# Optimization experiments

Hardware: AMD Instinct MI355X
Metric: run time of the kernel (lower is better)

## Reference

```python
import jax, jax.numpy as jnp
import numpy as np

N_NODES = 50000
N_EDGES = 800000
IN_DIM = 128
HID = 128
EMB = 128
HORIZON = 64
ACT = 8
N_AGENTS = 1024


def setup_inputs() -> dict:
    key = jax.random.key(0)
    ks = jax.random.split(key, 16)
    sc = lambda fan_in: 1.0 / np.sqrt(fan_in)

    inp = {
        "node_features": jax.random.normal(ks[0], (N_NODES, IN_DIM), dtype=jnp.float32),
        "edge_index": jax.random.randint(ks[1], (2, N_EDGES), 0, N_NODES, dtype=jnp.int64),
        "agent_idx": jax.random.randint(ks[2], (N_AGENTS,), 0, N_NODES, dtype=jnp.int64),
        # GraphConv1: out = lin_rel(sum_j x_j) + lin_root(x); lin_root has no bias
        "W1_rel": jax.random.uniform(ks[3], (HID, IN_DIM), jnp.float32, -sc(IN_DIM), sc(IN_DIM)),
        "b1_rel": jax.random.uniform(ks[4], (HID,), jnp.float32, -sc(IN_DIM), sc(IN_DIM)),
        "W1_root": jax.random.uniform(ks[5], (HID, IN_DIM), jnp.float32, -sc(IN_DIM), sc(IN_DIM)),
        # GraphConv2
        "W2_rel": jax.random.uniform(ks[6], (EMB, HID), jnp.float32, -sc(HID), sc(HID)),
        "b2_rel": jax.random.uniform(ks[7], (EMB,), jnp.float32, -sc(HID), sc(HID)),
        "W2_root": jax.random.uniform(ks[8], (EMB, HID), jnp.float32, -sc(HID), sc(HID)),
        # Policy MLP: Linear(EMB,HID)-ReLU-Linear(HID,HID)-ReLU-Linear(HID,HORIZON*ACT)
        "Wp1": jax.random.uniform(ks[9], (HID, EMB), jnp.float32, -sc(EMB), sc(EMB)),
        "bp1": jax.random.uniform(ks[10], (HID,), jnp.float32, -sc(EMB), sc(EMB)),
        "Wp2": jax.random.uniform(ks[11], (HID, HID), jnp.float32, -sc(HID), sc(HID)),
        "bp2": jax.random.uniform(ks[12], (HID,), jnp.float32, -sc(HID), sc(HID)),
        "Wp3": jax.random.uniform(ks[13], (HORIZON * ACT, HID), jnp.float32, -sc(HID), sc(HID)),
        "bp3": jax.random.uniform(ks[14], (HORIZON * ACT,), jnp.float32, -sc(HID), sc(HID)),
    }
    return inp


def _graph_conv(x, src, dst, W_rel, b_rel, W_root):
    # aggregate neighbor features (sum over incoming edges), then linear
    aggr = jax.ops.segment_sum(x[src], dst, num_segments=N_NODES)  # [N, d_in]
    return aggr @ W_rel.T + b_rel + x @ W_root.T


def reference(node_features, edge_index, agent_idx,
              W1_rel, b1_rel, W1_root, W2_rel, b2_rel, W2_root,
              Wp1, bp1, Wp2, bp2, Wp3, bp3):
    src, dst = edge_index[0], edge_index[1]
    h = jax.nn.relu(_graph_conv(node_features, src, dst, W1_rel, b1_rel, W1_root))
    z = jax.nn.relu(_graph_conv(h, src, dst, W2_rel, b2_rel, W2_root))
    sel = z[agent_idx]  # [A, EMB]
    m = jax.nn.relu(sel @ Wp1.T + bp1)
    m = jax.nn.relu(m @ Wp2.T + bp2)
    traj = m @ Wp3.T + bp3
    return traj.reshape(-1, HORIZON, ACT)
```

## Files before the change

### kernel.cpp

```cpp
#include <hip/hip_runtime.h>

#define NN 50000
#define NE 800000
#define DIM 128
#define NB 196
#define BCAP 4800
#define K1B 100

typedef __attribute__((ext_vector_type(8))) short bf16x8;
typedef __attribute__((ext_vector_type(8))) unsigned short u16x8;
typedef __attribute__((ext_vector_type(4))) float f32x4;

__device__ __forceinline__ unsigned short f2bf(float f) {
    unsigned int u = __builtin_bit_cast(unsigned int, f);
    u += 0x7fffu + ((u >> 16) & 1u);
    return (unsigned short)(u >> 16);
}
__device__ __forceinline__ float bf2f(unsigned int lo16) {
    return __builtin_bit_cast(float, lo16 << 16);
}

__global__ __launch_bounds__(256)
void cvt_all_kernel(const float* __restrict__ x, unsigned short* __restrict__ xb,
                    const float* __restrict__ s0, const float* __restrict__ s1,
                    const float* __restrict__ s2, const float* __restrict__ s3,
                    unsigned short* __restrict__ d0, unsigned short* __restrict__ d1,
                    unsigned short* __restrict__ d2, unsigned short* __restrict__ d3,
                    int* __restrict__ bcursor) {
    const int blk = blockIdx.x;
    const float* s;
    unsigned short* d;
    int base;
    if (blk < 3125) {
        s = x; d = xb;
        base = (blk * 256 + threadIdx.x) * 8;
    } else {
        int wb = blk - 3125;
        if (wb == 0 && threadIdx.x < NB) bcursor[threadIdx.x] = 0;
        int which = wb >> 3;
        s = which == 0 ? s0 : which == 1 ? s1 : which == 2 ? s2 : s3;
        d = which == 0 ? d0 : which == 1 ? d1 : which == 2 ? d2 : d3;
        base = ((wb & 7) * 256 + threadIdx.x) * 8;
    }
    float4 a = *(const float4*)(s + base);
    float4 b = *(const float4*)(s + base + 4);
    u16x8 r;
    r[0] = f2bf(a.x); r[1] = f2bf(a.y); r[2] = f2bf(a.z); r[3] = f2bf(a.w);
    r[4] = f2bf(b.x); r[5] = f2bf(b.y); r[6] = f2bf(b.z); r[7] = f2bf(b.w);
    *(u16x8*)(d + base) = r;
}

__global__ __launch_bounds__(256)
void bucket_kernel(const int* __restrict__ src, const int* __restrict__ dst,
                   int* __restrict__ bcursor, unsigned int* __restrict__ bedge) {
    __shared__ int hist[NB];
    __shared__ int base[NB];
    const int t = threadIdx.x;
    const int e0 = blockIdx.x * (NE / K1B);
    const int e1 = e0 + (NE / K1B);
    for (int i = t; i < NB; i += 256) hist[i] = 0;
    __syncthreads();
    for (int e = e0 + t; e < e1; e += 256)
        atomicAdd(&hist[dst[e] >> 8], 1);
    __syncthreads();
    for (int i = t; i < NB; i += 256) {
        base[i] = atomicAdd(&bcursor[i], hist[i]);
        hist[i] = 0;
    }
    __syncthreads();
    for (int e = e0 + t; e < e1; e += 256) {
        int d = dst[e];
        int b = d >> 8;
        int pos = base[b] + atomicAdd(&hist[b], 1);
        if (pos < BCAP)
            bedge[(size_t)b * BCAP + pos] = ((unsigned int)(d & 255) << 16) | (unsigned int)src[e];
    }
}

__global__ __launch_bounds__(256)
void bucket_csr_kernel(const int* __restrict__ bcursor,
                       const unsigned int* __restrict__ bedge,
                       int* __restrict__ eid, int2* __restrict__ off2) {
    __shared__ int cnt[256], start[256], run[256], s[256];
    const int b = blockIdx.x;
    const int t = threadIdx.x;
    int n = bcursor[b];
    if (n > BCAP) n = BCAP;
    cnt[t] = 0; run[t] = 0;
    __syncthreads();
    const unsigned int* be = bedge + (size_t)b * BCAP;
    for (int i = t; i < n; i += 256)
        atomicAdd(&cnt[be[i] >> 16], 1);
    __syncthreads();
    int v = cnt[t];
    s[t] = v;
#pragma unroll
    for (int d = 1; d < 256; d <<= 1) {
        __syncthreads();
        int tmp = (t >= d) ? s[t - d] : 0;
        __syncthreads();
        s[t] += tmp;
    }
    __syncthreads();
    int ex = s[t] - v;
    start[t] = ex;
    off2[b * 256 + t] = make_int2(b * BCAP + ex, b * BCAP + ex + v);
    __syncthreads();
    for (int i = t; i < n; i += 256) {
        unsigned int w = be[i];
        int node = w >> 16;
        int o = atomicAdd(&run[node], 1);
        eid[(size_t)b * BCAP + start[node] + o] = (int)(w & 0xffffu);
    }
}

__global__ __launch_bounds__(256)
void gather_bf16_kernel(const unsigned short* __restrict__ x,
                        const int2* __restrict__ off2,
                        const int* __restrict__ eid,
                        unsigned short* __restrict__ aggr) {
    const int node = blockIdx.x * 4 + (threadIdx.x >> 6);
    const int lane = threadIdx.x & 63;
    const int grp  = lane >> 4;
    const int c16  = lane & 15;
    const int2 se = off2[node];
    const int s = se.x, e = se.y;
    const unsigned short* __restrict__ xc = x + c16 * 8;
    float acc[8] = {0.f, 0.f, 0.f, 0.f, 0.f, 0.f, 0.f, 0.f};
    int i = s + grp;
    for (; i + 4 < e; i += 8) {
        int n0 = eid[i];
        int n1 = eid[i + 4];
        u16x8 v0 = *(const u16x8*)(xc + (size_t)n0 * DIM);
        u16x8 v1 = *(const u16x8*)(xc + (size_t)n1 * DIM);
#pragma unroll
        for (int j = 0; j < 8; ++j)
            acc[j] += bf2f((unsigned short)v0[j]) + bf2f((unsigned short)v1[j]);
    }
    if (i < e) {
        int n = eid[i];
        u16x8 v = *(const u16x8*)(xc + (size_t)n * DIM);
#pragma unroll
        for (int j = 0; j < 8; ++j) acc[j] += bf2f((unsigned short)v[j]);
    }
#pragma unroll
    for (int j = 0; j < 8; ++j) {
        acc[j] += __shfl_xor(acc[j], 16, 64);
        acc[j] += __shfl_xor(acc[j], 32, 64);
    }
    if (grp == 0) {
        u16x8 r;
#pragma unroll
        for (int j = 0; j < 8; ++j) r[j] = f2bf(acc[j]);
        *(u16x8*)(aggr + (size_t)node * DIM + c16 * 8) = r;
    }
}

__global__ __launch_bounds__(256)
void conv_mfma_kernel(const unsigned short* __restrict__ A0,
                      const unsigned short* __restrict__ A1,
                      const unsigned short* __restrict__ W0,
                      const unsigned short* __restrict__ W1,
                      const float* __restrict__ bias,
                      unsigned short* __restrict__ Out) {
    __shared__ __align__(16) unsigned short Wl[16384];
    const int tid = threadIdx.x;
    const int wave = tid >> 6;
    const int lane = tid & 63;
    const int m0 = blockIdx.x * 64 + wave * 16;
    const bool active = m0 < NN;
    const int col = lane & 15;
    const int kgrp = lane >> 4;
    const int swz = (col & 7) << 4;

    f32x4 acc[8];
#pragma unroll
    for (int t = 0; t < 8; ++t) acc[t] = (f32x4){0.f, 0.f, 0.f, 0.f};

    for (int mat = 0; mat < 2; ++mat) {
        const unsigned short* A = mat ? A1 : A0;
        const unsigned short* W = mat ? W1 : W0;
        __syncthreads();
#pragma unroll
        for (int i = 0; i < 8; ++i) {
            int chunk = i * 256 + tid;
            int row = chunk >> 4;
            int b = (chunk * 16) ^ ((row & 7) << 4);
            *(uint4*)((char*)Wl + b) = *(const uint4*)(W + chunk * 8);
        }
        __syncthreads();
        if (active) {
            const int arow = m0 + col;
#pragma unroll
            for (int ks = 0; ks < 4; ++ks) {
                bf16x8 afrag = *(const bf16x8*)(A + (size_t)arow * DIM + ks * 32 + kgrp * 8);
                const int kb = ks * 64 + kgrp * 16;
#pragma unroll
                for (int t = 0; t < 8; ++t) {
                    int n = t * 16 + col;
                    int byteoff = (n * 256 + kb) ^ swz;
                    bf16x8 bfrag = *(const bf16x8*)((const char*)Wl + byteoff);
                    acc[t] = __builtin_amdgcn_mfma_f32_16x16x32_bf16(afrag, bfrag, acc[t], 0, 0, 0);
                }
            }
        }
    }
    if (active) {
        const int rgrp = lane >> 4;
#pragma unroll
        for (int t = 0; t < 8; ++t) {
            int n = t * 16 + col;
            float bv = bias[n];
#pragma unroll
            for (int j = 0; j < 4; ++j) {
                float v = fmaxf(acc[t][j] + bv, 0.f);
                int row = m0 + rgrp * 4 + j;
                Out[(size_t)row * DIM + n] = f2bf(v);
            }
        }
    }
}

__global__ __launch_bounds__(256)
void mlp_kernel(const unsigned short* __restrict__ Z,
                const int* __restrict__ agent_idx,
                const float* __restrict__ Wp1, const float* __restrict__ bp1,
                const float* __restrict__ Wp2, const float* __restrict__ bp2,
                const float* __restrict__ Wp3, const float* __restrict__ bp3,
                float* __restrict__ Out) {
    __shared__ __align__(16) float sel[8][132];
    __shared__ __align__(16) float m1[8][132];
    __shared__ __align__(16) float m2[8][132];
    const int tid = threadIdx.x;
    const int ab = blockIdx.x * 8;

    {
        int al = tid >> 5;
        int c = (tid & 31) * 4;
        int node = agent_idx[ab + al];
        ushort4 v = *(const ushort4*)(Z + (size_t)node * DIM + c);
        sel[al][c + 0] = bf2f(v.x); sel[al][c + 1] = bf2f(v.y);
        sel[al][c + 2] = bf2f(v.z); sel[al][c + 3] = bf2f(v.w);
    }
    __syncthreads();
    {
        int o = tid & 127;
        int g = tid >> 7;
        float acc[4] = {0.f, 0.f, 0.f, 0.f};
        for (int k = 0; k < 128; k += 4) {
            float4 w = *(const float4*)(Wp1 + (size_t)o * 128 + k);
#pragma unroll
            for (int a = 0; a < 4; ++a) {
                int aa = g * 4 + a;
                acc[a] += w.x * sel[aa][k] + w.y * sel[aa][k + 1]
                        + w.z * sel[aa][k + 2] + w.w * sel[aa][k + 3];
            }
        }
        float b = bp1[o];
#pragma unroll
        for (int a = 0; a < 4; ++a) m1[g * 4 + a][o] = fmaxf(acc[a] + b, 0.f);
    }
    __syncthreads();
    {
        int o = tid & 127;
        int g = tid >> 7;
        float acc[4] = {0.f, 0.f, 0.f, 0.f};
        for (int k = 0; k < 128; k += 4) {
            float4 w = *(const float4*)(Wp2 + (size_t)o * 128 + k);
#pragma unroll
            for (int a = 0; a < 4; ++a) {
                int aa = g * 4 + a;
                acc[a] += w.x * m1[aa][k] + w.y * m1[aa][k + 1]
                        + w.z * m1[aa][k + 2] + w.w * m1[aa][k + 3];
            }
        }
        float b = bp2[o];
#pragma unroll
        for (int a = 0; a < 4; ++a) m2[g * 4 + a][o] = fmaxf(acc[a] + b, 0.f);
    }
    __syncthreads();
    {
#pragma unroll
        for (int oo = 0; oo < 2; ++oo) {
            int o = tid + oo * 256;
            float acc[8] = {0.f, 0.f, 0.f, 0.f, 0.f, 0.f, 0.f, 0.f};
            for (int k = 0; k < 128; k += 4) {
                float4 w = *(const float4*)(Wp3 + (size_t)o * 128 + k);
#pragma unroll
                for (int a = 0; a < 8; ++a) {
                    acc[a] += w.x * m2[a][k] + w.y * m2[a][k + 1]
                            + w.z * m2[a][k + 2] + w.w * m2[a][k + 3];
                }
            }
            float b = bp3[o];
#pragma unroll
            for (int a = 0; a < 8; ++a)
                Out[(size_t)(ab + a) * 512 + o] = acc[a] + b;
        }
    }
}

extern "C" void kernel_launch(void* const* d_in, const int* in_sizes, int n_in,
                              void* d_out, int out_size, void* d_ws, size_t ws_size,
                              hipStream_t stream) {
    const float* x       = (const float*)d_in[0];
    const int*   edge    = (const int*)d_in[1];
    const int*   src     = edge;
    const int*   dst     = edge + NE;
    const int*   agent   = (const int*)d_in[2];
    const float* W1_rel  = (const float*)d_in[3];
    const float* b1_rel  = (const float*)d_in[4];
    const float* W1_root = (const float*)d_in[5];
    const float* W2_rel  = (const float*)d_in[6];
    const float* b2_rel  = (const float*)d_in[7];
    const float* W2_root = (const float*)d_in[8];
    const float* Wp1     = (const float*)d_in[9];
    const float* bp1     = (const float*)d_in[10];
    const float* Wp2     = (const float*)d_in[11];
    const float* bp2     = (const float*)d_in[12];
    const float* Wp3     = (const float*)d_in[13];
    const float* bp3     = (const float*)d_in[14];
    float* out = (float*)d_out;

    const size_t NNDIM = (size_t)NN * DIM;
    unsigned short* xb  = (unsigned short*)d_ws;
    unsigned short* ab  = xb + NNDIM;
    unsigned short* hb  = ab + NNDIM;
    unsigned short* zb  = hb + NNDIM;
    unsigned short* w1r = zb + NNDIM;
    unsigned short* w1o = w1r + 16384;
    unsigned short* w2r = w1o + 16384;
    unsigned short* w2o = w2r + 16384;
    int2* off2          = (int2*)(w2o + 16384);
    int* bcursor        = (int*)(off2 + NB * 256);
    unsigned int* bedge = (unsigned int*)(bcursor + 200);
    int* eid            = (int*)(bedge + (size_t)NB * BCAP);

    const int conv_blocks = (NN + 63) / 64;
    const int gather_blocks = NN / 4;

    cvt_all_kernel<<<3157, 256, 0, stream>>>(x, xb, W1_rel, W1_root, W2_rel, W2_root,
                                             w1r, w1o, w2r, w2o, bcursor);

    bucket_kernel<<<K1B, 256, 0, stream>>>(src, dst, bcursor, bedge);
    bucket_csr_kernel<<<NB, 256, 0, stream>>>(bcursor, bedge, eid, off2);

    gather_bf16_kernel<<<gather_blocks, 256, 0, stream>>>(xb, off2, eid, ab);
    conv_mfma_kernel<<<conv_blocks, 256, 0, stream>>>(ab, xb, w1r, w1o, b1_rel, hb);
    gather_bf16_kernel<<<gather_blocks, 256, 0, stream>>>(hb, off2, eid, ab);
    conv_mfma_kernel<<<conv_blocks, 256, 0, stream>>>(ab, hb, w2r, w2o, b2_rel, zb);
    mlp_kernel<<<1024 / 8, 256, 0, stream>>>(zb, agent, Wp1, bp1, Wp2, bp2, Wp3, bp3, out);
}
```

Before: 153.4 us.

## Split bucketing into histogram, scan, scatter; fuse histogram into convert; unroll gather

The per-block dst histogram now runs as extra blocks of the conversion kernel, so it overlaps the bf16 conversion. A small wave-scan kernel then computes deterministic per-block bucket bases, and a separate scatter kernel places the edges. This removes the global atomics on bcursor and the serial histogram pass inside the bucket kernel. The gather loop is also unrolled to four edges per iteration to raise memory-level parallelism. The cost is one extra kernel launch plus an extra counts/bases buffer round trip.

Measured after the change: 160.1 us. +4.4%, slower.

```diff
diff --git a/kernel.cpp b/kernel.cpp
--- a/kernel.cpp
+++ b/kernel.cpp
@@ -6,6 +6,7 @@
 #define NB 196
 #define BCAP 4800
 #define K1B 100
+#define CVT_BLOCKS 3157
 
 typedef __attribute__((ext_vector_type(8))) short bf16x8;
 typedef __attribute__((ext_vector_type(8))) unsigned short u16x8;
@@ -21,26 +22,40 @@
 }
 
 __global__ __launch_bounds__(256)
-void cvt_all_kernel(const float* __restrict__ x, unsigned short* __restrict__ xb,
-                    const float* __restrict__ s0, const float* __restrict__ s1,
-                    const float* __restrict__ s2, const float* __restrict__ s3,
-                    unsigned short* __restrict__ d0, unsigned short* __restrict__ d1,
-                    unsigned short* __restrict__ d2, unsigned short* __restrict__ d3,
-                    int* __restrict__ bcursor) {
+void cvt_hist_kernel(const float* __restrict__ x, unsigned short* __restrict__ xb,
+                     const float* __restrict__ s0, const float* __restrict__ s1,
+                     const float* __restrict__ s2, const float* __restrict__ s3,
+                     unsigned short* __restrict__ d0, unsigned short* __restrict__ d1,
+                     unsigned short* __restrict__ d2, unsigned short* __restrict__ d3,
+                     const int* __restrict__ dst, int* __restrict__ counts) {
+    __shared__ int hist[NB];
     const int blk = blockIdx.x;
+    const int t = threadIdx.x;
+    if (blk >= CVT_BLOCKS) {
+        const int hb = blk - CVT_BLOCKS;
+        for (int i = t; i < NB; i += 256) hist[i] = 0;
+        __syncthreads();
+        const int e0 = hb * (NE / K1B);
+        const int e1 = e0 + (NE / K1B);
+        for (int e = e0 + t; e < e1; e += 256)
+            atomicAdd(&hist[dst[e] >> 8], 1);
+        __syncthreads();
+        for (int b = t; b < NB; b += 256)
+            counts[b * 128 + hb] = hist[b];
+        return;
+    }
     const float* s;
     unsigned short* d;
     int base;
     if (blk < 3125) {
         s = x; d = xb;
-        base = (blk * 256 + threadIdx.x) * 8;
+        base = (blk * 256 + t) * 8;
     } else {
         int wb = blk - 3125;
-        if (wb == 0 && threadIdx.x < NB) bcursor[threadIdx.x] = 0;
         int which = wb >> 3;
         s = which == 0 ? s0 : which == 1 ? s1 : which == 2 ? s2 : s3;
         d = which == 0 ? d0 : which == 1 ? d1 : which == 2 ? d2 : d3;
-        base = ((wb & 7) * 256 + threadIdx.x) * 8;
+        base = ((wb & 7) * 256 + t) * 8;
     }
     float4 a = *(const float4*)(s + base);
     float4 b = *(const float4*)(s + base + 4);
@@ -51,27 +66,48 @@
 }
 
 __global__ __launch_bounds__(256)
-void bucket_kernel(const int* __restrict__ src, const int* __restrict__ dst,
-                   int* __restrict__ bcursor, unsigned int* __restrict__ bedge) {
-    __shared__ int hist[NB];
-    __shared__ int base[NB];
+void scan_bases_kernel(const int* __restrict__ counts, int* __restrict__ bases,
+                       int* __restrict__ bcursor) {
+    const int wave = threadIdx.x >> 6;
+    const int lane = threadIdx.x & 63;
+    const int b = blockIdx.x * 4 + wave;
+    const int* c = counts + b * 128;
+    int v0 = c[lane];
+    int v1 = (lane < K1B - 64) ? c[64 + lane] : 0;
+    int s0 = v0;
+#pragma unroll
+    for (int d = 1; d < 64; d <<= 1) {
+        int tmp = __shfl_up(s0, d, 64);
+        if (lane >= d) s0 += tmp;
+    }
+    int total0 = __shfl(s0, 63, 64);
+    int s1 = v1;
+#pragma unroll
+    for (int d = 1; d < 64; d <<= 1) {
+        int tmp = __shfl_up(s1, d, 64);
+        if (lane >= d) s1 += tmp;
+    }
+    s1 += total0;
+    int total = __shfl(s1, K1B - 64 - 1, 64);
+    bases[b * 128 + lane] = s0 - v0;
+    if (lane < K1B - 64) bases[b * 128 + 64 + lane] = s1 - v1;
+    if (lane == 0) bcursor[b] = total;
+}
+
+__global__ __launch_bounds__(256)
+void scatter_kernel(const int* __restrict__ src, const int* __restrict__ dst,
+                    const int* __restrict__ bases, unsigned int* __restrict__ bedge) {
+    __shared__ int cur[NB];
     const int t = threadIdx.x;
-    const int e0 = blockIdx.x * (NE / K1B);
+    const int blk = blockIdx.x;
+    for (int b = t; b < NB; b += 256) cur[b] = bases[b * 128 + blk];
+    __syncthreads();
+    const int e0 = blk * (NE / K1B);
     const int e1 = e0 + (NE / K1B);
-    for (int i = t; i < NB; i += 256) hist[i] = 0;
-    __syncthreads();
-    for (int e = e0 + t; e < e1; e += 256)
-        atomicAdd(&hist[dst[e] >> 8], 1);
-    __syncthreads();
-    for (int i = t; i < NB; i += 256) {
-        base[i] = atomicAdd(&bcursor[i], hist[i]);
-        hist[i] = 0;
-    }
-    __syncthreads();
     for (int e = e0 + t; e < e1; e += 256) {
         int d = dst[e];
         int b = d >> 8;
-        int pos = base[b] + atomicAdd(&hist[b], 1);
+        int pos = atomicAdd(&cur[b], 1);
         if (pos < BCAP)
             bedge[(size_t)b * BCAP + pos] = ((unsigned int)(d & 255) << 16) | (unsigned int)src[e];
     }
@@ -128,9 +164,19 @@
     const unsigned short* __restrict__ xc = x + c16 * 8;
     float acc[8] = {0.f, 0.f, 0.f, 0.f, 0.f, 0.f, 0.f, 0.f};
     int i = s + grp;
+    for (; i + 12 < e; i += 16) {
+        int n0 = eid[i], n1 = eid[i + 4], n2 = eid[i + 8], n3 = eid[i + 12];
+        u16x8 v0 = *(const u16x8*)(xc + (size_t)n0 * DIM);
+        u16x8 v1 = *(const u16x8*)(xc + (size_t)n1 * DIM);
+        u16x8 v2 = *(const u16x8*)(xc + (size_t)n2 * DIM);
+        u16x8 v3 = *(const u16x8*)(xc + (size_t)n3 * DIM);
+#pragma unroll
+        for (int j = 0; j < 8; ++j)
+            acc[j] += (bf2f((unsigned short)v0[j]) + bf2f((unsigned short)v1[j]))
+                    + (bf2f((unsigned short)v2[j]) + bf2f((unsigned short)v3[j]));
+    }
     for (; i + 4 < e; i += 8) {
-        int n0 = eid[i];
-        int n1 = eid[i + 4];
+        int n0 = eid[i], n1 = eid[i + 4];
         u16x8 v0 = *(const u16x8*)(xc + (size_t)n0 * DIM);
         u16x8 v1 = *(const u16x8*)(xc + (size_t)n1 * DIM);
 #pragma unroll
@@ -333,16 +379,19 @@
     unsigned short* w2o = w2r + 16384;
     int2* off2          = (int2*)(w2o + 16384);
     int* bcursor        = (int*)(off2 + NB * 256);
-    unsigned int* bedge = (unsigned int*)(bcursor + 200);
+    int* counts         = bcursor + 200;
+    int* bases          = counts + NB * 128;
+    unsigned int* bedge = (unsigned int*)(bases + NB * 128);
     int* eid            = (int*)(bedge + (size_t)NB * BCAP);
 
     const int conv_blocks = (NN + 63) / 64;
     const int gather_blocks = NN / 4;
 
-    cvt_all_kernel<<<3157, 256, 0, stream>>>(x, xb, W1_rel, W1_root, W2_rel, W2_root,
-                                             w1r, w1o, w2r, w2o, bcursor);
-
-    bucket_kernel<<<K1B, 256, 0, stream>>>(src, dst, bcursor, bedge);
+    cvt_hist_kernel<<<CVT_BLOCKS + K1B, 256, 0, stream>>>(
+        x, xb, W1_rel, W1_root, W2_rel, W2_root, w1r, w1o, w2r, w2o, dst, counts);
+
+    scan_bases_kernel<<<NB / 4, 256, 0, stream>>>(counts, bases, bcursor);
+    scatter_kernel<<<K1B, 256, 0, stream>>>(src, dst, bases, bedge);
     bucket_csr_kernel<<<NB, 256, 0, stream>>>(bcursor, bedge, eid, off2);
 
     gather_bf16_kernel<<<gather_blocks, 256, 0, stream>>>(xb, off2, eid, ab);
```
